# Performance work log

Measured on AMD Instinct MI355X. Metric: run time of the kernel, lower is better.

Reference implementation:

```python
import jax, jax.numpy as jnp
import numpy as np

B, T, H, D = 256, 128, 256, 256
N_SUB = 2  # fixed-step RK4 substeps per observation interval (replaces adaptive odeint)


def setup_inputs() -> dict:
    key = jax.random.key(0)
    ks = jax.random.split(key, 16)
    # timestamps: strictly increasing, shared across batch (torch code uses b[0,:,0])
    times = jnp.cumsum(jax.random.uniform(ks[0], (T,), minval=0.05, maxval=0.15)) + 0.1
    vals = jax.random.uniform(ks[1], (B, T))
    b = jnp.stack([jnp.broadcast_to(times, (B, T)), vals], axis=-1)  # (B,T,2)
    u = jax.random.uniform(ks[2], (B, T))
    train_m = (u < 0.4).astype(jnp.float32)
    test_m = ((u >= 0.4) & (u < 0.7)).astype(jnp.float32)
    m = train_m + test_m  # disjoint -> in {0,1}
    h0 = jnp.zeros((B, H), jnp.float32)
    s = 0.05
    p = lambda k, shp: jax.random.normal(k, shp, jnp.float32) * s
    return {
        'b': b, 'm': m, 'train_m': train_m, 'test_m': test_m, 'h0': h0,
        # ODE func: Linear(H->D) then Linear(D->H) then tanh
        'W1': p(ks[3], (D, H)), 'b1': p(ks[4], (D,)),
        'W2': p(ks[5], (H, D)), 'b2': p(ks[6], (H,)),
        # GRUCell(input_size=1, hidden=H), torch layout (3H, in)
        'W_ih': p(ks[7], (3 * H, 1)), 'W_hh': p(ks[8], (3 * H, H)),
        'b_ih': p(ks[9], (3 * H,)), 'b_hh': p(ks[10], (3 * H,)),
        # output heads: Linear(H->D), Linear(D->1), tanh
        'Wo1': p(ks[11], (D, H)), 'bo1': p(ks[12], (D,)),
        'Wo2': p(ks[13], (1, D)), 'bo2': p(ks[14], (1,)),
    }


def _gru(x, h, W_ih, W_hh, b_ih, b_hh):
    gi = x @ W_ih.T + b_ih          # (B, 3H)
    gh = h @ W_hh.T + b_hh          # (B, 3H)
    i_r, i_z, i_n = jnp.split(gi, 3, axis=-1)
    h_r, h_z, h_n = jnp.split(gh, 3, axis=-1)
    r = jax.nn.sigmoid(i_r + h_r)
    z = jax.nn.sigmoid(i_z + h_z)
    n = jnp.tanh(i_n + r * h_n)
    return (1.0 - z) * n + z * h


def _ode_rnn(b, m, train_m, test_m, h0, W1, b1, W2, b2,
             W_ih, W_hh, b_ih, b_hh, Wo1, bo1, Wo2, bo2):
    f = lambda x: jnp.tanh((x @ W1.T + b1) @ W2.T + b2)  # autonomous ODE func

    def rk4(h, t0, t1):
        dt = (t1 - t0) / N_SUB
        def sub(h, _):
            k1 = f(h)
            k2 = f(h + 0.5 * dt * k1)
            k3 = f(h + 0.5 * dt * k2)
            k4 = f(h + dt * k3)
            return h + (dt / 6.0) * (k1 + 2.0 * k2 + 2.0 * k3 + k4), None
        h, _ = jax.lax.scan(sub, h, None, length=N_SUB)
        return h

    times = b[0, :, 0]                                      # (T,)
    t0s = jnp.concatenate([jnp.zeros((1,), times.dtype), times[:-1]])
    vals = b[:, :, 1]                                       # (B,T)

    def step(h, inp):
        t0, t1, bv, mv, trm, tem = inp
        hp = rk4(h, t0, t1)                                 # (B,H)
        out = jnp.tanh((hp @ Wo1.T + bo1) @ Wo2.T + bo2)[:, 0]  # (B,)
        htrain = _gru((bv * trm)[:, None], hp, W_ih, W_hh, b_ih, b_hh)
        htest = _gru((out * tem)[:, None], hp, W_ih, W_hh, b_ih, b_hh)
        h_new = trm[:, None] * htrain + tem[:, None] * htest + (1.0 - mv)[:, None] * hp
        return h_new, out

    xs = (t0s, times, vals.T, m.T, train_m.T, test_m.T)
    _, outs = jax.lax.scan(step, h0, xs)                    # outs: (T,B)
    return outs.T                                           # (B,T)


def reference(b, m, train_m, test_m, h0, W1, b1, W2, b2,
              W_ih, W_hh, b_ih, b_hh, Wo1, bo1, Wo2, bo2):
    return _ode_rnn(b, m, train_m, test_m, h0, W1, b1, W2, b2,
                    W_ih, W_hh, b_ih, b_hh, Wo1, bo1, Wo2, bo2)
```

## Files before the change

kernel.cpp:

```cpp
#include <hip/hip_runtime.h>

#define H 256
#define T_STEPS 128
#define B_BATCH 256
#define I_LDS 48
#define N_P16 104
#define XGRP 36

#define LOG2E 1.4426950408889634f

union CVH { unsigned int u; _Float16 h[2]; };

__device__ __forceinline__ float fexp2_(float x) {
#if __has_builtin(__builtin_amdgcn_exp2f)
    return __builtin_amdgcn_exp2f(x);
#else
    return exp2f(x);
#endif
}
__device__ __forceinline__ float frcp_(float x) {
#if __has_builtin(__builtin_amdgcn_rcpf)
    float r = __builtin_amdgcn_rcpf(x);
    return r * (2.0f - x * r);
#else
    return 1.0f / x;
#endif
}
__device__ __forceinline__ float tanhf_(float x) {
    float xc = fminf(fmaxf(x, -16.f), 16.f);
    float t  = fexp2_(xc * (2.f * LOG2E));
    return (t - 1.f) * frcp_(t + 1.f);
}
__device__ __forceinline__ float sigmoidf_(float x) {
    float xc = fminf(fmaxf(x, -30.f), 30.f);
    return frcp_(1.f + fexp2_(-xc * LOG2E));
}


__global__ void prep_weff(const float* __restrict__ W1, const float* __restrict__ W2,
                          const float* __restrict__ b1, const float* __restrict__ b2,
                          float* __restrict__ Weff, float* __restrict__ beff) {
    int i = blockIdx.x, j = threadIdx.x;
    const float* w2row = W2 + j * H;
    float acc = 0.f;
    for (int d = 0; d < H; ++d) acc += W1[d * H + i] * w2row[d];
    Weff[i * H + j] = acc;
    if (i == 0) {
        float bacc = b2[j];
        for (int d = 0; d < H; ++d) bacc += b1[d] * w2row[d];
        beff[j] = bacc;
    }
}

__global__ void prep_weffh16(const float* __restrict__ Weff, unsigned int* __restrict__ W16) {
    int idx = blockIdx.x * 1024 + threadIdx.x;
    int row = idx >> 7, jp = idx & 127;
    CVH cv;
    cv.h[0] = (_Float16)Weff[row * H + 2 * jp];
    cv.h[1] = (_Float16)Weff[row * H + 2 * jp + 1];
    W16[idx] = cv.u;
}

__global__ void prep_whht(const float* __restrict__ Whh, float* __restrict__ WhhT) {
    int idx = blockIdx.x * blockDim.x + threadIdx.x;
    int i = idx / 768;
    int r = idx - i * 768;
    WhhT[idx] = Whh[r * H + i];
}

__global__ void prep_whh16(const float* __restrict__ WhhT, unsigned int* __restrict__ W16) {
    int idx = blockIdx.x * blockDim.x + threadIdx.x;
    if (idx >= N_P16 * 768) return;
    int i2 = idx / 768;
    int r  = idx - i2 * 768;
    CVH cv;
    cv.h[0] = (_Float16)WhhT[(I_LDS + 2 * i2) * 768 + r];
    cv.h[1] = (_Float16)WhhT[(I_LDS + 2 * i2 + 1) * 768 + r];
    W16[idx] = cv.u;
}

__global__ void prep_wo(const float* __restrict__ Wo1, const float* __restrict__ Wo2,
                        const float* __restrict__ bo1, const float* __restrict__ bo2,
                        float* __restrict__ wo, float* __restrict__ bo) {
    int i = threadIdx.x;
    float acc = 0.f;
    for (int d = 0; d < H; ++d) acc += Wo1[d * H + i] * Wo2[d];
    wo[i] = acc;
    float p = bo1[i] * Wo2[i];
    __shared__ float red[4];
    for (int off = 32; off > 0; off >>= 1) p += __shfl_down(p, off);
    if ((i & 63) == 0) red[i >> 6] = p;
    __syncthreads();
    if (i == 0) bo[0] = red[0] + red[1] + red[2] + red[3] + bo2[0];
}


__global__ __attribute__((amdgpu_flat_work_group_size(1024, 1024),
                          amdgpu_waves_per_eu(4, 4)))
void ode_rnn_main(
    const float* __restrict__ b_in, const float* __restrict__ m_in,
    const float* __restrict__ trm_in, const float* __restrict__ tem_in,
    const float* __restrict__ h0,
    const unsigned int* __restrict__ WeffH16, const float* __restrict__ beff,
    const float* __restrict__ WhhT, const unsigned int* __restrict__ Whh16,
    const float* __restrict__ W_ih, const float* __restrict__ b_ih,
    const float* __restrict__ b_hh,
    const float* __restrict__ wo, const float* __restrict__ bo_p,
    float* __restrict__ out)
{
    const int tid = threadIdx.x;
    const int bb  = blockIdx.x;
    const int jp  = tid >> 3;
    const int e   = tid & 7;
    const int c   = e & 1;
    const int jc  = 2 * jp + c;

    __shared__ float whh_lds[I_LDS * 768];
    __shared__ __align__(16) float xsb[2][8 * XGRP];
    __shared__ __align__(16) float xsf[H];
    __shared__ float gh_lds[768];
    __shared__ float red[4];
    __shared__ float times_s[T_STEPS];
    __shared__ float bv_s[T_STEPS], trm_s[T_STEPS], tem_s[T_STEPS], m_s[T_STEPS];

    unsigned int wregh[32];
    #pragma unroll
    for (int il = 0; il < 32; ++il)
        wregh[il] = WeffH16[(32 * e + il) * 128 + jp];
    #pragma unroll
    for (int il = 0; il < 32; ++il)
        asm volatile("" : "+v"(wregh[il]));

    for (int k = tid; k < I_LDS * 768; k += 1024) whh_lds[k] = WhhT[k];
    if (tid < T_STEPS) {
        times_s[tid] = b_in[2 * tid];
        int bt = bb * T_STEPS + tid;
        bv_s[tid]  = b_in[2 * bt + 1];
        trm_s[tid] = trm_in[bt];
        tem_s[tid] = tem_in[bt];
        m_s[tid]   = m_in[bt];
    }

    float h = h0[bb * H + jc];
    const float be   = beff[jc];
    const float bihr = b_ih[jc], bihz = b_ih[H + jc], bihn = b_ih[2 * H + jc];
    const float bhhr = b_hh[jc], bhhz = b_hh[H + jc], bhhn = b_hh[2 * H + jc];
    const float wihr = W_ih[jc], wihz = W_ih[H + jc], wihn = W_ih[2 * H + jc];
    const float bo   = bo_p[0];
    const float wo_t = (tid >= 768) ? wo[tid - 768] : 0.f;

    const int pubpos = (jc >> 5) * XGRP + (jc & 31);

    if (e < 2) xsb[0][pubpos] = h;
    __syncthreads();

    #define EVAL(KOUT_) do {                                       \
        const float* xp_ = &xsb[cur][e * XGRP];                    \
        float a0_ = 0.f, a1_ = 0.f, b0_ = 0.f, b1_ = 0.f;          \
        _Pragma("unroll")                                          \
        for (int g_ = 0; g_ < 8; ++g_) {                           \
            float4 x_ = ((const float4*)xp_)[g_];                  \
            CVH w0_, w1_, w2_, w3_;                                \
            w0_.u = wregh[4 * g_ + 0];                             \
            w1_.u = wregh[4 * g_ + 1];                             \
            w2_.u = wregh[4 * g_ + 2];                             \
            w3_.u = wregh[4 * g_ + 3];                             \
            a0_ = fmaf((float)w0_.h[0], x_.x, a0_);                \
            b0_ = fmaf((float)w0_.h[1], x_.x, b0_);                \
            a1_ = fmaf((float)w1_.h[0], x_.y, a1_);                \
            b1_ = fmaf((float)w1_.h[1], x_.y, b1_);                \
            a0_ = fmaf((float)w2_.h[0], x_.z, a0_);                \
            b0_ = fmaf((float)w2_.h[1], x_.z, b0_);                \
            a1_ = fmaf((float)w3_.h[0], x_.w, a1_);                \
            b1_ = fmaf((float)w3_.h[1], x_.w, b1_);                \
        }                                                          \
        float s0_ = a0_ + a1_, s1_ = b0_ + b1_;                    \
        float v_ = (c == 0) ? s0_ : s1_;                           \
        float u_ = (c == 0) ? s1_ : s0_;                           \
        v_ += __shfl_xor(u_, 1);                                   \
        v_ += __shfl_xor(v_, 2);                                   \
        v_ += __shfl_xor(v_, 4);                                   \
        KOUT_ = tanhf_(be + v_);                                   \
    } while (0)

    #define PUBLISH(V_) do {                                       \
        if (e < 2) xsb[cur ^ 1][pubpos] = (V_);                    \
        __syncthreads();                                           \
        cur ^= 1;                                                  \
    } while (0)

    float tprev = 0.f;
    #pragma unroll 1
    for (int t = 0; t < T_STEPS; ++t) {
        float t1 = times_s[t];
        float dt = (t1 - tprev) * 0.5f;
        tprev = t1;

        int cur = 0;
        float k1, k2, k3, k4;
        #pragma unroll 1
        for (int s = 0; s < 2; ++s) {
            EVAL(k1); PUBLISH(fmaf(0.5f * dt, k1, h));
            EVAL(k2); PUBLISH(fmaf(0.5f * dt, k2, h));
            EVAL(k3); PUBLISH(fmaf(dt, k3, h));
            EVAL(k4);
            h = fmaf(dt * (1.f / 6.f), k1 + 2.f * (k2 + k3) + k4, h);
            if (s == 0) PUBLISH(h);
        }

        if (e < 2) xsf[jc] = h;
        __syncthreads();

        if (tid < 768) {
            float c0 = 0.f, c1 = 0.f, c2 = 0.f, c3 = 0.f;
            const unsigned int* wp = Whh16 + tid;
            #pragma unroll 13
            for (int ii = 0; ii < N_P16; ii += 2) {
                float4 xv = *(const float4*)(xsf + I_LDS + 2 * ii);
                CVH ca, cb;
                ca.u = wp[ii * 768];
                cb.u = wp[(ii + 1) * 768];
                c0 = fmaf(xv.x, (float)ca.h[0], c0);
                c1 = fmaf(xv.y, (float)ca.h[1], c1);
                c2 = fmaf(xv.z, (float)cb.h[0], c2);
                c3 = fmaf(xv.w, (float)cb.h[1], c3);
            }
            float g0 = 0.f, g1 = 0.f, g2 = 0.f, g3 = 0.f;
            const float* wl = whh_lds + tid;
            #pragma unroll 4
            for (int i = 0; i < I_LDS; i += 4) {
                float4 xv = *(const float4*)(xsf + i);
                g0 = fmaf(xv.x, wl[(i + 0) * 768], g0);
                g1 = fmaf(xv.y, wl[(i + 1) * 768], g1);
                g2 = fmaf(xv.z, wl[(i + 2) * 768], g2);
                g3 = fmaf(xv.w, wl[(i + 3) * 768], g3);
            }
            gh_lds[tid] = ((c0 + c1) + (c2 + c3)) + ((g0 + g1) + (g2 + g3));
        } else {
            float p = xsf[tid - 768] * wo_t;
            #pragma unroll
            for (int off = 32; off > 0; off >>= 1) p += __shfl_down(p, off);
            if ((tid & 63) == 0) red[(tid - 768) >> 6] = p;
        }
        __syncthreads();

        {
            float outv = tanhf_(red[0] + red[1] + red[2] + red[3] + bo);
            float bv = bv_s[t], trm = trm_s[t], tem = tem_s[t], mv = m_s[t];
            float ghr = gh_lds[jc] + bhhr;
            float ghz = gh_lds[256 + jc] + bhhz;
            float ghn = gh_lds[512 + jc] + bhhn;
            float x1v = bv * trm, x2v = outv * tem;

            float r1 = sigmoidf_(fmaf(x1v, wihr, bihr) + ghr);
            float z1 = sigmoidf_(fmaf(x1v, wihz, bihz) + ghz);
            float n1 = tanhf_(fmaf(x1v, wihn, bihn) + r1 * ghn);
            float h1 = (1.f - z1) * n1 + z1 * h;

            float r2 = sigmoidf_(fmaf(x2v, wihr, bihr) + ghr);
            float z2 = sigmoidf_(fmaf(x2v, wihz, bihz) + ghz);
            float n2 = tanhf_(fmaf(x2v, wihn, bihn) + r2 * ghn);
            float h2 = (1.f - z2) * n2 + z2 * h;

            if (tid == 0) out[bb * T_STEPS + t] = outv;
            h = trm * h1 + tem * h2 + (1.f - mv) * h;
        }

        if (e < 2) xsb[0][pubpos] = h;
        __syncthreads();
    }
    #undef EVAL
    #undef PUBLISH
}


extern "C" void kernel_launch(void* const* d_in, const int* in_sizes, int n_in,
                              void* d_out, int out_size, void* d_ws, size_t ws_size,
                              hipStream_t stream) {
    const float* b_in = (const float*)d_in[0];
    const float* m_in = (const float*)d_in[1];
    const float* trm  = (const float*)d_in[2];
    const float* tem  = (const float*)d_in[3];
    const float* h0   = (const float*)d_in[4];
    const float* W1   = (const float*)d_in[5];
    const float* b1   = (const float*)d_in[6];
    const float* W2   = (const float*)d_in[7];
    const float* b2   = (const float*)d_in[8];
    const float* W_ih = (const float*)d_in[9];
    const float* W_hh = (const float*)d_in[10];
    const float* b_ih = (const float*)d_in[11];
    const float* b_hh = (const float*)d_in[12];
    const float* Wo1  = (const float*)d_in[13];
    const float* bo1  = (const float*)d_in[14];
    const float* Wo2  = (const float*)d_in[15];
    const float* bo2  = (const float*)d_in[16];

    float* ws = (float*)d_ws;
    float*        Weff    = ws;
    float*        beff    = Weff + 65536;
    float*        WhhT    = beff + 256;
    float*        wo      = WhhT + 196608;
    float*        bo      = wo + 256;
    unsigned int* Whh16   = (unsigned int*)(bo + 1);
    unsigned int* WeffH16 = Whh16 + 79872;

    prep_weff<<<256, 256, 0, stream>>>(W1, W2, b1, b2, Weff, beff);
    prep_weffh16<<<32, 1024, 0, stream>>>(Weff, WeffH16);
    prep_whht<<<192, 1024, 0, stream>>>(W_hh, WhhT);
    prep_whh16<<<78, 1024, 0, stream>>>(WhhT, Whh16);
    prep_wo<<<1, 256, 0, stream>>>(Wo1, Wo2, bo1, bo2, wo, bo);

    ode_rnn_main<<<B_BATCH, 1024, 0, stream>>>(b_in, m_in, trm, tem, h0,
                                               WeffH16, beff, WhhT, Whh16,
                                               W_ih, b_ih, b_hh, wo, bo,
                                               (float*)d_out);
}
```

Baseline: 2.092 ms.

## Halve workgroup to 512 threads with 64 register weights per thread, drop LDS Whh cache

Shrinks the block from 1024 to 512 threads. Each thread now holds 64 packed fp16 Weff words in registers and reduces across 4 lanes instead of 8. The 48-row fp32 Whh slice in LDS is removed, so the whole GRU hidden matvec streams fp16 Whh from global memory/cache, with some threads walking two output columns. The aim is fewer threads per barrier, a shorter shuffle reduction and a lighter LDS footprint. The cost is more register pressure, a longer serial per-thread chain for the ODE and GH matvecs, and more global weight traffic.

```diff
diff --git a/kernel.cpp b/kernel.cpp
--- a/kernel.cpp
+++ b/kernel.cpp
@@ -3,9 +3,7 @@
 #define H 256
 #define T_STEPS 128
 #define B_BATCH 256
-#define I_LDS 48
-#define N_P16 104
-#define XGRP 36
+#define XGRP2 68
 
 #define LOG2E 1.4426950408889634f
 
@@ -68,14 +66,13 @@
     WhhT[idx] = Whh[r * H + i];
 }
 
-__global__ void prep_whh16(const float* __restrict__ WhhT, unsigned int* __restrict__ W16) {
+__global__ void prep_whh16f(const float* __restrict__ WhhT, unsigned int* __restrict__ W16) {
     int idx = blockIdx.x * blockDim.x + threadIdx.x;
-    if (idx >= N_P16 * 768) return;
     int i2 = idx / 768;
     int r  = idx - i2 * 768;
     CVH cv;
-    cv.h[0] = (_Float16)WhhT[(I_LDS + 2 * i2) * 768 + r];
-    cv.h[1] = (_Float16)WhhT[(I_LDS + 2 * i2 + 1) * 768 + r];
+    cv.h[0] = (_Float16)WhhT[(2 * i2) * 768 + r];
+    cv.h[1] = (_Float16)WhhT[(2 * i2 + 1) * 768 + r];
     W16[idx] = cv.u;
 }
 
@@ -95,14 +92,14 @@
 }
 
 
-__global__ __attribute__((amdgpu_flat_work_group_size(1024, 1024),
+__global__ __attribute__((amdgpu_flat_work_group_size(512, 512),
                           amdgpu_waves_per_eu(4, 4)))
 void ode_rnn_main(
     const float* __restrict__ b_in, const float* __restrict__ m_in,
     const float* __restrict__ trm_in, const float* __restrict__ tem_in,
     const float* __restrict__ h0,
     const unsigned int* __restrict__ WeffH16, const float* __restrict__ beff,
-    const float* __restrict__ WhhT, const unsigned int* __restrict__ Whh16,
+    const unsigned int* __restrict__ Whh16f,
     const float* __restrict__ W_ih, const float* __restrict__ b_ih,
     const float* __restrict__ b_hh,
     const float* __restrict__ wo, const float* __restrict__ bo_p,
@@ -110,28 +107,26 @@
 {
     const int tid = threadIdx.x;
     const int bb  = blockIdx.x;
-    const int jp  = tid >> 3;
-    const int e   = tid & 7;
+    const int jp  = tid >> 2;
+    const int e   = tid & 3;
     const int c   = e & 1;
     const int jc  = 2 * jp + c;
 
-    __shared__ float whh_lds[I_LDS * 768];
-    __shared__ __align__(16) float xsb[2][8 * XGRP];
+    __shared__ __align__(16) float xsb[2][4 * XGRP2];
     __shared__ __align__(16) float xsf[H];
     __shared__ float gh_lds[768];
     __shared__ float red[4];
     __shared__ float times_s[T_STEPS];
     __shared__ float bv_s[T_STEPS], trm_s[T_STEPS], tem_s[T_STEPS], m_s[T_STEPS];
 
-    unsigned int wregh[32];
+    unsigned int wregh[64];
     #pragma unroll
-    for (int il = 0; il < 32; ++il)
-        wregh[il] = WeffH16[(32 * e + il) * 128 + jp];
+    for (int il = 0; il < 64; ++il)
+        wregh[il] = WeffH16[(64 * e + il) * 128 + jp];
     #pragma unroll
-    for (int il = 0; il < 32; ++il)
+    for (int il = 0; il < 64; ++il)
         asm volatile("" : "+v"(wregh[il]));
 
-    for (int k = tid; k < I_LDS * 768; k += 1024) whh_lds[k] = WhhT[k];
     if (tid < T_STEPS) {
         times_s[tid] = b_in[2 * tid];
         int bt = bb * T_STEPS + tid;
@@ -147,18 +142,18 @@
     const float bhhr = b_hh[jc], bhhz = b_hh[H + jc], bhhn = b_hh[2 * H + jc];
     const float wihr = W_ih[jc], wihz = W_ih[H + jc], wihn = W_ih[2 * H + jc];
     const float bo   = bo_p[0];
-    const float wo_t = (tid >= 768) ? wo[tid - 768] : 0.f;
-
-    const int pubpos = (jc >> 5) * XGRP + (jc & 31);
+    const float wo_t = (tid >= 256) ? wo[tid - 256] : 0.f;
+
+    const int pubpos = (jc >> 6) * XGRP2 + (jc & 63);
 
     if (e < 2) xsb[0][pubpos] = h;
     __syncthreads();
 
     #define EVAL(KOUT_) do {                                       \
-        const float* xp_ = &xsb[cur][e * XGRP];                    \
+        const float* xp_ = &xsb[cur][e * XGRP2];                   \
         float a0_ = 0.f, a1_ = 0.f, b0_ = 0.f, b1_ = 0.f;          \
         _Pragma("unroll")                                          \
-        for (int g_ = 0; g_ < 8; ++g_) {                           \
+        for (int g_ = 0; g_ < 16; ++g_) {                          \
             float4 x_ = ((const float4*)xp_)[g_];                  \
             CVH w0_, w1_, w2_, w3_;                                \
             w0_.u = wregh[4 * g_ + 0];                             \
@@ -179,7 +174,6 @@
         float u_ = (c == 0) ? s1_ : s0_;                           \
         v_ += __shfl_xor(u_, 1);                                   \
         v_ += __shfl_xor(v_, 2);                                   \
-        v_ += __shfl_xor(v_, 4);                                   \
         KOUT_ = tanhf_(be + v_);                                   \
     } while (0)
 
@@ -187,6 +181,23 @@
         if (e < 2) xsb[cur ^ 1][pubpos] = (V_);                    \
         __syncthreads();                                           \
         cur ^= 1;                                                  \
+    } while (0)
+
+    #define GH_WALK(O_, DST_) do {                                 \
+        const unsigned int* wp_ = Whh16f + (O_);                   \
+        float c0_ = 0.f, c1_ = 0.f, c2_ = 0.f, c3_ = 0.f;          \
+        _Pragma("unroll 16")                                       \
+        for (int ii_ = 0; ii_ < 128; ii_ += 2) {                   \
+            float4 xv_ = *(const float4*)(xsf + 2 * ii_);          \
+            CVH ca_, cb_;                                          \
+            ca_.u = wp_[ii_ * 768];                                \
+            cb_.u = wp_[(ii_ + 1) * 768];                          \
+            c0_ = fmaf(xv_.x, (float)ca_.h[0], c0_);               \
+            c1_ = fmaf(xv_.y, (float)ca_.h[1], c1_);               \
+            c2_ = fmaf(xv_.z, (float)cb_.h[0], c2_);               \
+            c3_ = fmaf(xv_.w, (float)cb_.h[1], c3_);               \
+        }                                                          \
+        DST_ = (c0_ + c1_) + (c2_ + c3_);                          \
     } while (0)
 
     float tprev = 0.f;
@@ -211,36 +222,20 @@
         if (e < 2) xsf[jc] = h;
         __syncthreads();
 
-        if (tid < 768) {
-            float c0 = 0.f, c1 = 0.f, c2 = 0.f, c3 = 0.f;
-            const unsigned int* wp = Whh16 + tid;
-            #pragma unroll 13
-            for (int ii = 0; ii < N_P16; ii += 2) {
-                float4 xv = *(const float4*)(xsf + I_LDS + 2 * ii);
-                CVH ca, cb;
-                ca.u = wp[ii * 768];
-                cb.u = wp[(ii + 1) * 768];
-                c0 = fmaf(xv.x, (float)ca.h[0], c0);
-                c1 = fmaf(xv.y, (float)ca.h[1], c1);
-                c2 = fmaf(xv.z, (float)cb.h[0], c2);
-                c3 = fmaf(xv.w, (float)cb.h[1], c3);
-            }
-            float g0 = 0.f, g1 = 0.f, g2 = 0.f, g3 = 0.f;
-            const float* wl = whh_lds + tid;
-            #pragma unroll 4
-            for (int i = 0; i < I_LDS; i += 4) {
-                float4 xv = *(const float4*)(xsf + i);
-                g0 = fmaf(xv.x, wl[(i + 0) * 768], g0);
-                g1 = fmaf(xv.y, wl[(i + 1) * 768], g1);
-                g2 = fmaf(xv.z, wl[(i + 2) * 768], g2);
-                g3 = fmaf(xv.w, wl[(i + 3) * 768], g3);
-            }
-            gh_lds[tid] = ((c0 + c1) + (c2 + c3)) + ((g0 + g1) + (g2 + g3));
+        {
+            float ga;
+            GH_WALK(tid, ga);
+            gh_lds[tid] = ga;
+        }
+        if (tid < 256) {
+            float gb;
+            GH_WALK(512 + tid, gb);
+            gh_lds[512 + tid] = gb;
         } else {
-            float p = xsf[tid - 768] * wo_t;
+            float p = xsf[tid - 256] * wo_t;
             #pragma unroll
             for (int off = 32; off > 0; off >>= 1) p += __shfl_down(p, off);
-            if ((tid & 63) == 0) red[(tid - 768) >> 6] = p;
+            if ((tid & 63) == 0) red[(tid - 256) >> 6] = p;
         }
         __syncthreads();
 
@@ -271,6 +266,7 @@
     }
     #undef EVAL
     #undef PUBLISH
+    #undef GH_WALK
 }
 
 
@@ -301,17 +297,17 @@
     float*        WhhT    = beff + 256;
     float*        wo      = WhhT + 196608;
     float*        bo      = wo + 256;
-    unsigned int* Whh16   = (unsigned int*)(bo + 1);
-    unsigned int* WeffH16 = Whh16 + 79872;
+    unsigned int* Whh16f  = (unsigned int*)(bo + 1);
+    unsigned int* WeffH16 = Whh16f + 98304;
 
     prep_weff<<<256, 256, 0, stream>>>(W1, W2, b1, b2, Weff, beff);
     prep_weffh16<<<32, 1024, 0, stream>>>(Weff, WeffH16);
     prep_whht<<<192, 1024, 0, stream>>>(W_hh, WhhT);
-    prep_whh16<<<78, 1024, 0, stream>>>(WhhT, Whh16);
+    prep_whh16f<<<96, 1024, 0, stream>>>(WhhT, Whh16f);
     prep_wo<<<1, 256, 0, stream>>>(Wo1, Wo2, bo1, bo2, wo, bo);
 
-    ode_rnn_main<<<B_BATCH, 1024, 0, stream>>>(b_in, m_in, trm, tem, h0,
-                                               WeffH16, beff, WhhT, Whh16,
-                                               W_ih, b_ih, b_hh, wo, bo,
-                                               (float*)d_out);
-}
+    ode_rnn_main<<<B_BATCH, 512, 0, stream>>>(b_in, m_in, trm, tem, h0,
+                                              WeffH16, beff, Whh16f,
+                                              W_ih, b_ih, b_hh, wo, bo,
+                                              (float*)d_out);
+}
```

Result: slower. 7.206 ms (+244.5%).
